# Kernel tuning notes

Measured on AMD Instinct MI355X. Metric: run time of the kernel, lower is better.

The kernel has to match this reference:

```python
import jax, jax.numpy as jnp
import numpy as np

B, L = 8, 2048
D_MODEL = 512
D_TYPE = 32
NUM_TYPES = 20
REG = 5.0          # regulizing_param
BETAS = (0.4, 0.3, 1.0)
EPS = 1e-6


def setup_inputs() -> dict:
    key = jax.random.key(0)
    ks = jax.random.split(key, 9)
    event_type = jax.random.randint(ks[0], (B, L), 0, NUM_TYPES + 1)  # 0 = padding idx
    event_time = jax.random.uniform(ks[1], (B, L), dtype=jnp.float32)
    arrival_times = jax.random.uniform(ks[2], (B, L), dtype=jnp.float32)
    # BiasedPositionalEmbedding: Wt = Linear(1, d_model//2, bias=False) -> weight vector [d/2]
    Wt_pos = jax.random.normal(ks[3], (D_MODEL // 2,), dtype=jnp.float32) * 0.02
    # type embedding table, padding_idx=0 row zeroed
    type_emb = jax.random.normal(ks[4], (NUM_TYPES + 1, D_TYPE), dtype=jnp.float32) * 0.02
    type_emb = type_emb.at[0].set(0.0)
    # magic_kernel params: linear maps on concat([xd_bar, xd]) (2*d_type) -> lengthscale / gate
    w_l = jax.random.normal(ks[5], (2 * D_TYPE,), dtype=jnp.float32) * 0.1
    b_l = jnp.float32(0.5)
    w_g = jax.random.normal(ks[6], (2 * D_TYPE,), dtype=jnp.float32) * 0.1
    b_g = jnp.float32(0.0)
    return {"event_type": event_type, "event_time": event_time,
            "arrival_times": arrival_times, "Wt_pos": Wt_pos, "type_emb": type_emb,
            "w_l": w_l, "b_l": b_l, "w_g": w_g, "b_g": b_g}


def _biased_pos_emb(event_time, Wt_pos):
    # phi = Wt(interval.unsqueeze(-1)) : [B,L,d/2]
    phi = event_time[..., None] * Wt_pos  # outer product with weight column
    position = jnp.arange(L, dtype=jnp.float32)[:, None]                     # [L,1]
    div_term = jnp.exp(jnp.arange(0, D_MODEL, 2, dtype=jnp.float32)
                       * (-np.log(10000.0) / D_MODEL))                       # [d/2]
    arc = (position * div_term)[None]                                        # [1,L,d/2]
    return jnp.concatenate([jnp.sin(arc + phi), jnp.cos(arc + phi)], axis=-1)  # [B,L,d]


def reference(event_type, event_time, arrival_times, Wt_pos, type_emb, w_l, b_l, w_g, b_g):
    temp_enc = _biased_pos_emb(event_time, Wt_pos)          # [B,L,d_model]
    te = type_emb[event_type]                               # [B,L,d_type]
    hidden_vector = jnp.concatenate([temp_enc, te], -1)     # num_types > 1 branch

    # pairwise time differences: xt_bar[b,i,j]=t[b,j], xt[b,i,j]=t[b,i]
    t_diff = jnp.abs(event_time[:, None, :] - event_time[:, :, None])  # [B,L,L]

    # magic_kernel on concat([xd_bar, xd]) without materializing [B,L,L,2*d_type]:
    # Linear(concat) = te[b,j] @ w[:d_type] + te[b,i] @ w[d_type:] + bias
    pa = te @ w_l[:D_TYPE]   # [B,L] (j-side)
    pb = te @ w_l[D_TYPE:]   # [B,L] (i-side)
    ga = te @ w_g[:D_TYPE]
    gb = te @ w_g[D_TYPE:]
    l = jax.nn.softplus(pa[:, None, :] + pb[:, :, None] + b_l) + EPS   # lengthscale [B,L,L]
    g = jax.nn.sigmoid(REG * (ga[:, None, :] + gb[:, :, None] + b_g))  # gate [B,L,L]
    k_se = jnp.exp(-(t_diff * t_diff) / (2.0 * l * l))
    k_ex = jnp.exp(-t_diff / l)
    scores = g * (BETAS[0] * k_se + BETAS[1] * k_ex) * BETAS[2]

    # subsequent mask: (triu(ones, 0) - 1)^2 -> 1 strictly below diagonal, 0 elsewhere;
    # masked_fill where mask==0 with 0 (softmax=False default)
    keep = jnp.tril(jnp.ones((L, L), dtype=bool), -1)[None]  # [1,L,L]
    scores = jnp.where(keep, scores, 0.0)
    return (scores, hidden_vector, t_diff)
```

## Files before the change

### kernel.cpp

```cpp
#include <hip/hip_runtime.h>
#include <stdint.h>

#define BB 8
#define LL 2048
#define DT 32
#define HID 544
#define REGP 5.0f
#define BETA0 0.4f
#define BETA1 0.3f
#define EPSV 1e-6f

__global__ __launch_bounds__(256) void prep_k(
    const int* __restrict__ etype, const float* __restrict__ etime,
    const float* __restrict__ wtpos, const float* __restrict__ temb,
    const float* __restrict__ wl, const float* __restrict__ wg,
    const float* __restrict__ blp, const float* __restrict__ bgp,
    float* __restrict__ hidden,
    float* __restrict__ pa, float* __restrict__ pbl,
    float* __restrict__ ga5, float* __restrict__ gb5)
{
    const int row = blockIdx.x;
    const int i = row & (LL - 1);
    const int tid = threadIdx.x;
    const float t = etime[row];

    const float c = -0.03597789207803197f;
    float divt = expf((float)tid * c);
    float arc = fmaf((float)i, divt, t * wtpos[tid]);
    size_t hbase = (size_t)row * HID;
    hidden[hbase + tid]       = sinf(arc);
    hidden[hbase + 256 + tid] = cosf(arc);

    if (tid < 32) {
        int ty = etype[row];
        float te = temb[ty * DT + tid];
        hidden[hbase + 512 + tid] = te;
        float va = te * wl[tid];
        float vb = te * wl[32 + tid];
        float vc = te * wg[tid];
        float vd = te * wg[32 + tid];
        #pragma unroll
        for (int m = 16; m > 0; m >>= 1) {
            va += __shfl_xor(va, m, 64);
            vb += __shfl_xor(vb, m, 64);
            vc += __shfl_xor(vc, m, 64);
            vd += __shfl_xor(vd, m, 64);
        }
        if (tid == 0) {
            pa[row]  = va;
            pbl[row] = vb + blp[0];
            ga5[row] = -REGP * vc;
            gb5[row] = -REGP * (vd + bgp[0]);
        }
    }
}

__global__ __launch_bounds__(256) void pair_k(
    const float* __restrict__ etime,
    const float* __restrict__ pa, const float* __restrict__ pbl,
    const float* __restrict__ ga5, const float* __restrict__ gb5,
    float* __restrict__ scores, float* __restrict__ tdiff)
{
    const int b  = blockIdx.z;
    const int i0 = blockIdx.y << 3;
    const int j0 = (blockIdx.x << 10) + (threadIdx.x << 2);
    const int rowb = b * LL;

    const float4 tj = *(const float4*)(etime + rowb + j0);
    const float4 pj = *(const float4*)(pa + rowb + j0);
    const float4 gj = *(const float4*)(ga5 + rowb + j0);

    #pragma unroll
    for (int ii = 0; ii < 8; ++ii) {
        const int i = i0 + ii;
        const float ti  = etime[rowb + i];
        const float pbi = pbl[rowb + i];
        const float gbi = gb5[rowb + i];
        const size_t base = ((size_t)(rowb + i) << 11) + j0;

        float4 dd;
        dd.x = fabsf(tj.x - ti);
        dd.y = fabsf(tj.y - ti);
        dd.z = fabsf(tj.z - ti);
        dd.w = fabsf(tj.w - ti);
        *(float4*)(tdiff + base) = dd;

        float4 sc;
        if (j0 < i) {
            float pjv[4] = {pj.x, pj.y, pj.z, pj.w};
            float gjv[4] = {gj.x, gj.y, gj.z, gj.w};
            float dv[4]  = {dd.x, dd.y, dd.z, dd.w};
            float s[4];
            #pragma unroll
            for (int e = 0; e < 4; ++e) {
                float l  = __logf(1.0f + __expf(pjv[e] + pbi)) + EPSV;
                float rl = __builtin_amdgcn_rcpf(l);
                float u  = dv[e] * rl;
                float kse = __expf(-0.5f * u * u);
                float kex = __expf(-u);
                float g   = __builtin_amdgcn_rcpf(1.0f + __expf(gjv[e] + gbi));
                float v   = g * fmaf(BETA0, kse, BETA1 * kex);
                s[e] = ((j0 + e) < i) ? v : 0.0f;
            }
            sc.x = s[0]; sc.y = s[1]; sc.z = s[2]; sc.w = s[3];
        } else {
            sc.x = 0.0f; sc.y = 0.0f; sc.z = 0.0f; sc.w = 0.0f;
        }
        *(float4*)(scores + base) = sc;
    }
}

extern "C" void kernel_launch(void* const* d_in, const int* in_sizes, int n_in,
                              void* d_out, int out_size, void* d_ws, size_t ws_size,
                              hipStream_t stream) {
    const int*   etype = (const int*)d_in[0];
    const float* etime = (const float*)d_in[1];
    const float* wtpos = (const float*)d_in[3];
    const float* temb  = (const float*)d_in[4];
    const float* wl    = (const float*)d_in[5];
    const float* blp   = (const float*)d_in[6];
    const float* wg    = (const float*)d_in[7];
    const float* bgp   = (const float*)d_in[8];

    float* out    = (float*)d_out;
    float* scores = out;
    float* hidden = out + (size_t)BB * LL * LL;
    float* tdiff  = hidden + (size_t)BB * LL * HID;

    float* pa  = (float*)d_ws;
    float* pbl = pa + BB * LL;
    float* ga5 = pbl + BB * LL;
    float* gb5 = ga5 + BB * LL;

    prep_k<<<BB * LL, 256, 0, stream>>>(etype, etime, wtpos, temb, wl, wg,
                                        blp, bgp, hidden, pa, pbl, ga5, gb5);
    pair_k<<<dim3(2, LL / 8, BB), 256, 0, stream>>>(etime, pa, pbl, ga5, gb5,
                                                    scores, tdiff);
}
```

Before: 322.6 us.

## Use nontemporal stores, precompute exponentials per row, and enlarge per-block work

Output stores in both kernels become nontemporal so the large score, tdiff and hidden writes bypass cache retention. The per-row softplus and sigmoid inputs are pre-exponentiated in prep, so the pairwise kernel needs one fma instead of an exp for each of them. The prep kernel now handles 8 rows per block and the pair kernel 16 rows per block. The factored exponentials can overflow for large logits, which changes numerics in extreme cases.

```diff
diff --git a/kernel.cpp b/kernel.cpp
--- a/kernel.cpp
+++ b/kernel.cpp
@@ -10,82 +10,91 @@
 #define BETA1 0.3f
 #define EPSV 1e-6f
 
+typedef float v4 __attribute__((ext_vector_type(4)));
+
 __global__ __launch_bounds__(256) void prep_k(
     const int* __restrict__ etype, const float* __restrict__ etime,
     const float* __restrict__ wtpos, const float* __restrict__ temb,
     const float* __restrict__ wl, const float* __restrict__ wg,
     const float* __restrict__ blp, const float* __restrict__ bgp,
     float* __restrict__ hidden,
-    float* __restrict__ pa, float* __restrict__ pbl,
-    float* __restrict__ ga5, float* __restrict__ gb5)
+    float* __restrict__ paE, float* __restrict__ pbE,
+    float* __restrict__ gaE, float* __restrict__ gbE)
 {
-    const int row = blockIdx.x;
-    const int i = row & (LL - 1);
+    const int r0 = blockIdx.x << 3;
     const int tid = threadIdx.x;
-    const float t = etime[row];
+    const float c = -0.03597789207803197f;
+    const float divt = __expf((float)tid * c);
+    const float wt = wtpos[tid];
+    const float bl = blp[0];
+    const float bg = bgp[0];
 
-    const float c = -0.03597789207803197f;
-    float divt = expf((float)tid * c);
-    float arc = fmaf((float)i, divt, t * wtpos[tid]);
-    size_t hbase = (size_t)row * HID;
-    hidden[hbase + tid]       = sinf(arc);
-    hidden[hbase + 256 + tid] = cosf(arc);
+    #pragma unroll
+    for (int rr = 0; rr < 8; ++rr) {
+        const int row = r0 + rr;
+        const int i = row & (LL - 1);
+        const float t = etime[row];
+        float arc = fmaf((float)i, divt, t * wt);
+        size_t hbase = (size_t)row * HID;
+        __builtin_nontemporal_store(sinf(arc), hidden + hbase + tid);
+        __builtin_nontemporal_store(cosf(arc), hidden + hbase + 256 + tid);
 
-    if (tid < 32) {
-        int ty = etype[row];
-        float te = temb[ty * DT + tid];
-        hidden[hbase + 512 + tid] = te;
-        float va = te * wl[tid];
-        float vb = te * wl[32 + tid];
-        float vc = te * wg[tid];
-        float vd = te * wg[32 + tid];
-        #pragma unroll
-        for (int m = 16; m > 0; m >>= 1) {
-            va += __shfl_xor(va, m, 64);
-            vb += __shfl_xor(vb, m, 64);
-            vc += __shfl_xor(vc, m, 64);
-            vd += __shfl_xor(vd, m, 64);
-        }
-        if (tid == 0) {
-            pa[row]  = va;
-            pbl[row] = vb + blp[0];
-            ga5[row] = -REGP * vc;
-            gb5[row] = -REGP * (vd + bgp[0]);
+        if (tid < 32) {
+            int ty = etype[row];
+            float te = temb[ty * DT + tid];
+            __builtin_nontemporal_store(te, hidden + hbase + 512 + tid);
+            float va = te * wl[tid];
+            float vb = te * wl[32 + tid];
+            float vc = te * wg[tid];
+            float vd = te * wg[32 + tid];
+            #pragma unroll
+            for (int m = 16; m > 0; m >>= 1) {
+                va += __shfl_xor(va, m, 64);
+                vb += __shfl_xor(vb, m, 64);
+                vc += __shfl_xor(vc, m, 64);
+                vd += __shfl_xor(vd, m, 64);
+            }
+            if (tid == 0) {
+                paE[row] = __expf(va);
+                pbE[row] = __expf(vb + bl);
+                gaE[row] = __expf(-REGP * vc);
+                gbE[row] = __expf(-REGP * (vd + bg));
+            }
         }
     }
 }
 
 __global__ __launch_bounds__(256) void pair_k(
     const float* __restrict__ etime,
-    const float* __restrict__ pa, const float* __restrict__ pbl,
-    const float* __restrict__ ga5, const float* __restrict__ gb5,
+    const float* __restrict__ paE, const float* __restrict__ pbE,
+    const float* __restrict__ gaE, const float* __restrict__ gbE,
     float* __restrict__ scores, float* __restrict__ tdiff)
 {
     const int b  = blockIdx.z;
-    const int i0 = blockIdx.y << 3;
+    const int i0 = blockIdx.y << 4;
     const int j0 = (blockIdx.x << 10) + (threadIdx.x << 2);
     const int rowb = b * LL;
 
-    const float4 tj = *(const float4*)(etime + rowb + j0);
-    const float4 pj = *(const float4*)(pa + rowb + j0);
-    const float4 gj = *(const float4*)(ga5 + rowb + j0);
+    const v4 tj = *(const v4*)(etime + rowb + j0);
+    const v4 pj = *(const v4*)(paE + rowb + j0);
+    const v4 gj = *(const v4*)(gaE + rowb + j0);
 
-    #pragma unroll
-    for (int ii = 0; ii < 8; ++ii) {
+    #pragma unroll 4
+    for (int ii = 0; ii < 16; ++ii) {
         const int i = i0 + ii;
         const float ti  = etime[rowb + i];
-        const float pbi = pbl[rowb + i];
-        const float gbi = gb5[rowb + i];
+        const float pbi = pbE[rowb + i];
+        const float gbi = gbE[rowb + i];
         const size_t base = ((size_t)(rowb + i) << 11) + j0;
 
-        float4 dd;
+        v4 dd;
         dd.x = fabsf(tj.x - ti);
         dd.y = fabsf(tj.y - ti);
         dd.z = fabsf(tj.z - ti);
         dd.w = fabsf(tj.w - ti);
-        *(float4*)(tdiff + base) = dd;
+        __builtin_nontemporal_store(dd, (v4*)(tdiff + base));
 
-        float4 sc;
+        v4 sc;
         if (j0 < i) {
             float pjv[4] = {pj.x, pj.y, pj.z, pj.w};
             float gjv[4] = {gj.x, gj.y, gj.z, gj.w};
@@ -93,20 +102,20 @@
             float s[4];
             #pragma unroll
             for (int e = 0; e < 4; ++e) {
-                float l  = __logf(1.0f + __expf(pjv[e] + pbi)) + EPSV;
+                float l  = __logf(fmaf(pjv[e], pbi, 1.0f)) + EPSV;
                 float rl = __builtin_amdgcn_rcpf(l);
                 float u  = dv[e] * rl;
                 float kse = __expf(-0.5f * u * u);
                 float kex = __expf(-u);
-                float g   = __builtin_amdgcn_rcpf(1.0f + __expf(gjv[e] + gbi));
+                float g   = __builtin_amdgcn_rcpf(fmaf(gjv[e], gbi, 1.0f));
                 float v   = g * fmaf(BETA0, kse, BETA1 * kex);
                 s[e] = ((j0 + e) < i) ? v : 0.0f;
             }
             sc.x = s[0]; sc.y = s[1]; sc.z = s[2]; sc.w = s[3];
         } else {
-            sc.x = 0.0f; sc.y = 0.0f; sc.z = 0.0f; sc.w = 0.0f;
+            sc = (v4)(0.0f);
         }
-        *(float4*)(scores + base) = sc;
+        __builtin_nontemporal_store(sc, (v4*)(scores + base));
     }
 }
 
@@ -127,13 +136,13 @@
     float* hidden = out + (size_t)BB * LL * LL;
     float* tdiff  = hidden + (size_t)BB * LL * HID;
 
-    float* pa  = (float*)d_ws;
-    float* pbl = pa + BB * LL;
-    float* ga5 = pbl + BB * LL;
-    float* gb5 = ga5 + BB * LL;
+    float* paE = (float*)d_ws;
+    float* pbE = paE + BB * LL;
+    float* gaE = pbE + BB * LL;
+    float* gbE = gaE + BB * LL;
 
-    prep_k<<<BB * LL, 256, 0, stream>>>(etype, etime, wtpos, temb, wl, wg,
-                                        blp, bgp, hidden, pa, pbl, ga5, gb5);
-    pair_k<<<dim3(2, LL / 8, BB), 256, 0, stream>>>(etime, pa, pbl, ga5, gb5,
-                                                    scores, tdiff);
+    prep_k<<<BB * LL / 8, 256, 0, stream>>>(etype, etime, wtpos, temb, wl, wg,
+                                            blp, bgp, hidden, paE, pbE, gaE, gbE);
+    pair_k<<<dim3(2, LL / 16, BB), 256, 0, stream>>>(etime, paE, pbE, gaE, gbE,
+                                                     scores, tdiff);
 }
```

After: 327.3 us. About the same (+1.5%).
